# Kernel optimization log

Measured on AMD Instinct MI355X. Metric: run time of the kernel, lower is better.

The kernel has to match this reference:

```python
import jax, jax.numpy as jnp
import numpy as np

B, S, F, K = 64, 1024, 128, 64  # batch, seq(=l), feat(=d), bottleneck k


def setup_inputs() -> dict:
    key = jax.random.key(0)
    ks = jax.random.split(key, 24)
    r = lambda k_, sh, s=0.05: (jax.random.normal(k_, sh, dtype=jnp.float32) * s)
    inp = {
        'f1_norm': jax.random.normal(ks[0], (B, S, F), dtype=jnp.float32),
        'f2_norm': jax.random.normal(ks[1], (B, S, F), dtype=jnp.float32),
        'f3_norm': jax.random.normal(ks[2], (B, S, F), dtype=jnp.float32),
        # AMLP params (Linear(F, 2F))
        'Wi': r(ks[3], (2 * F, F)), 'bi': r(ks[4], (2 * F,)),
        'Wq': r(ks[5], (2 * F, F)), 'bq': r(ks[6], (2 * F,)),
        'Wvp': r(ks[7], (2 * F, F)), 'bvp': r(ks[8], (2 * F,)),
        # affine_{a,v,l}: Linear(l, l, bias=False) -> weight [l, l]
        'Aa': r(ks[9], (S, S)), 'Av': r(ks[10], (S, S)), 'Al': r(ks[11], (S, S)),
        # W_{a,v,t}: Linear(l, k) -> [k, l]
        'Wa': r(ks[12], (K, S)), 'Wv': r(ks[13], (K, S)), 'Wt': r(ks[14], (K, S)),
        # W_c{a,v,t}: Linear(2d, k) -> [k, 2F]
        'Wca': r(ks[15], (K, 2 * F)), 'Wcv': r(ks[16], (K, 2 * F)), 'Wct': r(ks[17], (K, 2 * F)),
        # W_h{a,v,t}: Linear(k, l) -> [l, k]
        'Wha': r(ks[18], (S, K)), 'Whv': r(ks[19], (S, K)), 'Wht': r(ks[20], (S, K)),
    }
    return inp


def _amlp(txt, aud, vis, Wi, bi, Wq, bq, Wvp, bvp):
    f1 = jnp.einsum('bsf,gf->bsg', txt, Wi) + bi  # [B,S,2F]
    f2 = jnp.einsum('bsf,gf->bsg', aud, Wq) + bq
    f3 = jnp.einsum('bsf,gf->bsg', vis, Wvp) + bvp
    n1 = jnp.linalg.norm(f1)
    n2 = jnp.linalg.norm(f2)
    n3 = jnp.linalg.norm(f3)
    # faithful to source: third term is scalar factor3 * norm3 (broadcast)
    exp_out = (n1 / (n1 + n2)) * f1 + (n2 / (n1 + n2)) * f2 + (n3 / (n1 + n2 + n3)) * n3
    b, s, g = exp_out.shape
    z = exp_out.reshape(b, s, g // 2, 2).sum(-1)  # AvgPool1d(2,2) * 2 == pair sum
    # F.normalize default dim=1 (over sequence axis for 3D tensor)
    z = z / jnp.maximum(jnp.linalg.norm(z, axis=1, keepdims=True), 1e-12)
    return z  # [B,S,F]


def reference(f1_norm, f2_norm, f3_norm, Wi, bi, Wq, bq, Wvp, bvp,
              Aa, Av, Al, Wa, Wv, Wt, Wca, Wcv, Wct, Wha, Whv, Wht):
    txt, aud, vis = f1_norm, f2_norm, f3_norm
    G = _amlp(txt, aud, vis, Wi, bi, Wq, bq, Wvp, bvp)  # [B,S,F]

    G_ag = jnp.concatenate([aud, G], axis=-1)  # [B,S,2F]
    G_vg = jnp.concatenate([vis, G], axis=-1)
    G_lg = jnp.concatenate([txt, G], axis=-1)
    scale = np.sqrt(G_ag.shape[-1]).astype(np.float32)  # sqrt(2F); same for all three

    # a_j = affine(G_xg^T); att = x^T @ a_j^T  ==  x^T @ (A @ G_xg)
    AGa = jnp.einsum('ts,bsc->btc', Aa, G_ag)
    C_a = jnp.tanh(jnp.einsum('bsf,bsc->bfc', aud, AGa) / scale)  # [B,F,2F]
    AGv = jnp.einsum('ts,bsc->btc', Av, G_ag)  # NOTE: source bug uses G_ag, not G_vg
    C_v = jnp.tanh(jnp.einsum('bsf,bsc->bfc', vis, AGv) / scale)
    AGl = jnp.einsum('ts,bsc->btc', Al, G_lg)
    C_t = jnp.tanh(jnp.einsum('bsf,bsc->bfc', txt, AGl) / scale)

    H_a = jax.nn.relu(jnp.einsum('bfc,kc->bfk', C_a, Wca) + jnp.einsum('bsf,ks->bfk', aud, Wa))
    H_v = jax.nn.relu(jnp.einsum('bfc,kc->bfk', C_v, Wcv) + jnp.einsum('bsf,ks->bfk', vis, Wv))
    H_t = jax.nn.relu(jnp.einsum('bfc,kc->bfk', C_t, Wct) + jnp.einsum('bsf,ks->bfk', txt, Wt))

    out_a = jnp.einsum('bfk,sk->bsf', H_a, Wha) + aud  # [B,S,F]
    out_v = jnp.einsum('bfk,sk->bsf', H_v, Whv) + vis
    out_t = jnp.einsum('bfk,sk->bsf', H_t, Wht) + txt
    return (out_t, out_a, out_v)
```

## Files before the change

### kernel.cpp

```cpp
#include <hip/hip_runtime.h>
#include <math.h>

constexpr int Bb = 64;
constexpr int Ss = 1024;
constexpr int Ff = 128;
constexpr int G2 = 256;
constexpr int Kk = 64;
constexpr int NE = 1152;

typedef __bf16 bfrag __attribute__((ext_vector_type(8)));
typedef float  facc  __attribute__((ext_vector_type(4)));
typedef short  s8v   __attribute__((ext_vector_type(8)));

__device__ __forceinline__ short f2bfs(float f) {
  union { float f; unsigned u; } v; v.f = f;
  unsigned r = v.u + 0x7FFFu + ((v.u >> 16) & 1u);
  return (short)(r >> 16);
}
__device__ __forceinline__ float bf2fs(short s) {
  union { unsigned u; float f; } v; v.u = ((unsigned)(unsigned short)s) << 16;
  return v.f;
}
__device__ __forceinline__ facc mfma16(bfrag a, bfrag b, facc c) {
  return __builtin_amdgcn_mfma_f32_16x16x32_bf16(a, b, c, 0, 0, 0);
}
__device__ __forceinline__ void gld16(const void* g, void* l) {
  __builtin_amdgcn_global_load_lds(
      (const __attribute__((address_space(1))) void*)g,
      (__attribute__((address_space(3))) void*)l, 16, 0, 0);
}

__global__ void k_transpose(const float* __restrict__ aud, const float* __restrict__ vis,
                            const float* __restrict__ txt, short* __restrict__ xT) {
  __shared__ float tile[64][65];
  int z = blockIdx.z;
  int mod = z >> 6, b = z & 63;
  const float* x = (mod == 0) ? aud : (mod == 1) ? vis : txt;
  int s0 = blockIdx.x * 64, f0 = blockIdx.y * 64;
  int tid = threadIdx.x;
  for (int i = 0; i < 16; ++i) {
    int idx = i * 256 + tid;
    int si = idx >> 6, fi = idx & 63;
    tile[si][fi] = x[((size_t)b * Ss + s0 + si) * Ff + f0 + fi];
  }
  __syncthreads();
  short* dst = xT + ((size_t)mod * Bb + b) * Ff * Ss;
  for (int i = 0; i < 16; ++i) {
    int idx = i * 256 + tid;
    int fi = idx >> 6, si = idx & 63;
    dst[(size_t)(f0 + fi) * Ss + s0 + si] = f2bfs(tile[si][fi]);
  }
}

__global__ void k_build_aextT(const float* __restrict__ Aa, const float* __restrict__ Av,
                              const float* __restrict__ Al, const float* __restrict__ Wa,
                              const float* __restrict__ Wv, const float* __restrict__ Wt,
                              short* __restrict__ aextT) {
  __shared__ float tile[64][65];
  int mod = blockIdx.z;
  const float* A = (mod == 0) ? Aa : (mod == 1) ? Av : Al;
  const float* W = (mod == 0) ? Wa : (mod == 1) ? Wv : Wt;
  short* dst = aextT + (size_t)mod * NE * Ss;
  int n0 = blockIdx.x * 64, t0 = blockIdx.y * 64;
  int tid = threadIdx.x;
  if (n0 < Ss) {
    for (int i = 0; i < 16; ++i) {
      int idx = i * 256 + tid;
      int ti = idx >> 6, nj = idx & 63;
      tile[ti][nj] = A[(size_t)(t0 + ti) * Ss + n0 + nj];
    }
    __syncthreads();
    for (int i = 0; i < 16; ++i) {
      int idx = i * 256 + tid;
      int nj = idx >> 6, ti = idx & 63;
      dst[(size_t)(n0 + nj) * Ss + t0 + ti] = f2bfs(tile[ti][nj]);
    }
  } else if (n0 < Ss + Kk) {
    for (int i = 0; i < 16; ++i) {
      int idx = i * 256 + tid;
      int j = idx >> 6, tt = idx & 63;
      dst[(size_t)(n0 + j) * Ss + t0 + tt] = f2bfs(W[(size_t)(n0 - Ss + j) * Ss + t0 + tt]);
    }
  } else {
    for (int i = 0; i < 16; ++i) {
      int idx = i * 256 + tid;
      int j = idx >> 6, tt = idx & 63;
      dst[(size_t)(n0 + j) * Ss + t0 + tt] = 0;
    }
  }
}

__global__ void k_build_w(const float* __restrict__ Wca, const float* __restrict__ Wcv,
                          const float* __restrict__ Wct, const float* __restrict__ Wha,
                          const float* __restrict__ Whv, const float* __restrict__ Wht,
                          const float* __restrict__ Wi, const float* __restrict__ Wq,
                          const float* __restrict__ Wvp,
                          short* __restrict__ wcb, short* __restrict__ whb,
                          short* __restrict__ wbar) {
  int idx = blockIdx.x * 256 + threadIdx.x;
  const int n1 = 3 * Kk * G2;
  const int n2 = n1 + 3 * Ss * Kk;
  if (idx < n1) {
    int mod = idx / (Kk * G2), r = idx - mod * (Kk * G2);
    const float* W = (mod == 0) ? Wca : (mod == 1) ? Wcv : Wct;
    wcb[idx] = f2bfs(W[r]);
  } else if (idx < n2) {
    int j = idx - n1;
    int mod = j / (Ss * Kk), r = j - mod * (Ss * Kk);
    const float* W = (mod == 0) ? Wha : (mod == 1) ? Whv : Wht;
    whb[j] = f2bfs(W[r]);
  } else {
    int j = idx - n2;
    int mod = j / (G2 * Ff), r = j - mod * (G2 * Ff);
    int n = r >> 7, k = r & 127;
    int t = n >> 4, nl = n & 15;
    int c = k >> 5, q = (k >> 3) & 3, e = k & 7;
    const float* W = (mod == 0) ? Wi : (mod == 1) ? Wq : Wvp;
    wbar[mod * G2 * Ff + (((t * 4 + c) * 64 + q * 16 + nl) * 8) + e] = f2bfs(W[r]);
  }
}

__global__ void __launch_bounds__(256, 3) k_amlp(
    const float* __restrict__ txt, const float* __restrict__ aud, const float* __restrict__ vis,
    const float* __restrict__ bi, const float* __restrict__ bq, const float* __restrict__ bvp,
    const short* __restrict__ wbar,
    short* __restrict__ p1, short* __restrict__ p2, float* __restrict__ sumsq) {
  int mod = blockIdx.y;
  const float* x    = (mod == 0) ? txt : (mod == 1) ? aud : vis;
  const float* bias = (mod == 0) ? bi  : (mod == 1) ? bq  : bvp;
  const short* wbm  = wbar + mod * G2 * Ff;
  short* pout = (mod == 0) ? p1 : (mod == 1) ? p2 : nullptr;

  __shared__ float wred[4];
  int tid = threadIdx.x, lane = tid & 63, wave = tid >> 6;
  int quad = lane >> 4, nl = lane & 15;

  bfrag wreg[4][4];
#pragma unroll
  for (int tt = 0; tt < 4; ++tt)
#pragma unroll
    for (int c = 0; c < 4; ++c)
      wreg[tt][c] = *(const bfrag*)(wbm + ((((wave * 4 + tt) * 4 + c) * 64 + lane) * 8));

  float bia[4];
#pragma unroll
  for (int tt = 0; tt < 4; ++tt) bia[tt] = bias[wave * 64 + tt * 16 + nl];

  const float* xblk = x + (size_t)(blockIdx.x * 256) * Ff;
  facc zero = {0.f, 0.f, 0.f, 0.f};
  float sq = 0.f;

  float4 buf[8];
  {
    const float* xrow = xblk + (size_t)nl * Ff;
#pragma unroll
    for (int c = 0; c < 4; ++c) {
      buf[c * 2]     = *(const float4*)(xrow + c * 32 + quad * 8);
      buf[c * 2 + 1] = *(const float4*)(xrow + c * 32 + quad * 8 + 4);
    }
  }

  for (int g = 0; g < 16; ++g) {
    bfrag af[4];
#pragma unroll
    for (int c = 0; c < 4; ++c) {
      float4 a0 = buf[c * 2], a1 = buf[c * 2 + 1];
      af[c][0] = (__bf16)a0.x; af[c][1] = (__bf16)a0.y;
      af[c][2] = (__bf16)a0.z; af[c][3] = (__bf16)a0.w;
      af[c][4] = (__bf16)a1.x; af[c][5] = (__bf16)a1.y;
      af[c][6] = (__bf16)a1.z; af[c][7] = (__bf16)a1.w;
    }
    if (g < 15) {
      const float* xrow = xblk + (size_t)((g + 1) * 16 + nl) * Ff;
#pragma unroll
      for (int c = 0; c < 4; ++c) {
        buf[c * 2]     = *(const float4*)(xrow + c * 32 + quad * 8);
        buf[c * 2 + 1] = *(const float4*)(xrow + c * 32 + quad * 8 + 4);
      }
    }
    facc acc[4];
#pragma unroll
    for (int tt = 0; tt < 4; ++tt) acc[tt] = zero;
#pragma unroll
    for (int c = 0; c < 4; ++c)
#pragma unroll
      for (int tt = 0; tt < 4; ++tt)
        acc[tt] = mfma16(af[c], wreg[tt][c], acc[tt]);

    int drow = blockIdx.x * 256 + g * 16 + quad * 4;
#pragma unroll
    for (int tt = 0; tt < 4; ++tt)
#pragma unroll
      for (int r = 0; r < 4; ++r) {
        float fv = acc[tt][r] + bia[tt];
        sq += fv * fv;
        if (pout) {
          float fo = fv + __shfl_xor(fv, 1, 64);
          if ((lane & 1) == 0)
            pout[(size_t)(drow + r) * Ff + wave * 32 + tt * 8 + (nl >> 1)] = f2bfs(fo);
        }
      }
  }
  for (int off = 32; off > 0; off >>= 1) sq += __shfl_down(sq, off, 64);
  if (lane == 0) wred[wave] = sq;
  __syncthreads();
  if (tid == 0) atomicAdd(&sumsq[mod], wred[0] + wred[1] + wred[2] + wred[3]);
}

__global__ void k_colnorm(const short* __restrict__ p1, const short* __restrict__ p2,
                          const float* __restrict__ sumsq, float* __restrict__ colnsq) {
  float n1 = sqrtf(sumsq[0]), n2 = sqrtf(sumsq[1]), n3 = sqrtf(sumsq[2]);
  float w1 = n1 / (n1 + n2), w2 = n2 / (n1 + n2);
  float tc = 2.f * n3 * n3 / (n1 + n2 + n3);
  int b = blockIdx.x, j = threadIdx.x;
  int s0 = blockIdx.y * 64;
  float a = 0.f;
  for (int s = s0; s < s0 + 64; ++s) {
    size_t off = ((size_t)b * Ss + s) * Ff + j;
    float z = w1 * bf2fs(p1[off]) + w2 * bf2fs(p2[off]) + tc;
    a += z * z;
  }
  atomicAdd(&colnsq[b * Ff + j], a);
}

__global__ void k_gnormT(const short* __restrict__ p1, const short* __restrict__ p2,
                         const float* __restrict__ sumsq, const float* __restrict__ colnsq,
                         short* __restrict__ gT) {
  __shared__ float tile[64][65];
  float n1 = sqrtf(sumsq[0]), n2 = sqrtf(sumsq[1]), n3 = sqrtf(sumsq[2]);
  float w1 = n1 / (n1 + n2), w2 = n2 / (n1 + n2);
  float tc = 2.f * n3 * n3 / (n1 + n2 + n3);
  int b = blockIdx.z, s0 = blockIdx.x * 64, f0 = blockIdx.y * 64;
  int tid = threadIdx.x;
  for (int i = 0; i < 16; ++i) {
    int idx = i * 256 + tid;
    int si = idx >> 6, fi = idx & 63;
    size_t off = ((size_t)b * Ss + s0 + si) * Ff + f0 + fi;
    float z = w1 * bf2fs(p1[off]) + w2 * bf2fs(p2[off]) + tc;
    float cn = fmaxf(sqrtf(colnsq[b * Ff + f0 + fi]), 1e-12f);
    tile[si][fi] = z / cn;
  }
  __syncthreads();
  short* dst = gT + (size_t)b * Ff * Ss;
  for (int i = 0; i < 16; ++i) {
    int idx = i * 256 + tid;
    int fi = idx >> 6, si = idx & 63;
    dst[(size_t)(f0 + fi) * Ss + s0 + si] = f2bfs(tile[si][fi]);
  }
}

__global__ void __launch_bounds__(256) k_mgemm(const short* __restrict__ xT,
                                               const short* __restrict__ aextT,
                                               short* __restrict__ mxext) {
  int mod = blockIdx.z;
  const short* Ap = xT + (size_t)mod * Bb * Ff * Ss;
  const short* Bp = aextT + (size_t)mod * NE * Ss;
  short* Op = mxext + (size_t)mod * Bb * Ff * NE;
  int M0 = blockIdx.x * 128, N0 = blockIdx.y * 128;
  __shared__ short As[128 * 64];
  __shared__ short Bs[128 * 64];
  int tid = threadIdx.x, lane = tid & 63, wave = tid >> 6;
  int quad = lane >> 4, nl = lane & 15;
  int wm = (wave >> 1) * 64, wn = (wave & 1) * 64;
  facc zero = {0.f, 0.f, 0.f, 0.f};
  facc acc[4][4];
  for (int i = 0; i < 4; ++i) for (int j = 0; j < 4; ++j) acc[i][j] = zero;
  for (int k0 = 0; k0 < Ss; k0 += 64) {
    __syncthreads();
#pragma unroll
    for (int i = 0; i < 4; ++i) {
      int idx = i * 256 + tid;
      int r = idx >> 3, cs = ((idx & 7) ^ (r & 7)) * 8;
      gld16(Ap + (size_t)(M0 + r) * Ss + k0 + cs, As + idx * 8);
      gld16(Bp + (size_t)(N0 + r) * Ss + k0 + cs, Bs + idx * 8);
    }
    __syncthreads();
#pragma unroll
    for (int kc = 0; kc < 2; ++kc) {
      bfrag a[4], bfr[4];
      for (int mt = 0; mt < 4; ++mt) {
        int row = wm + mt * 16 + nl;
        a[mt] = *(const bfrag*)(As + row * 64 + (((kc * 4 + quad) ^ (row & 7)) * 8));
      }
      for (int nt = 0; nt < 4; ++nt) {
        int row = wn + nt * 16 + nl;
        bfr[nt] = *(const bfrag*)(Bs + row * 64 + (((kc * 4 + quad) ^ (row & 7)) * 8));
      }
      for (int mt = 0; mt < 4; ++mt)
        for (int nt = 0; nt < 4; ++nt)
          acc[mt][nt] = mfma16(a[mt], bfr[nt], acc[mt][nt]);
    }
  }
  for (int mt = 0; mt < 4; ++mt)
    for (int nt = 0; nt < 4; ++nt)
      for (int r = 0; r < 4; ++r) {
        int row = M0 + wm + mt * 16 + quad * 4 + r;
        int col = N0 + wn + nt * 16 + nl;
        Op[(size_t)row * NE + col] = f2bfs(acc[mt][nt][r]);
      }
}

__global__ void __launch_bounds__(512) k_chgemm(const short* __restrict__ mxext,
                                                const short* __restrict__ xT,
                                                const short* __restrict__ gT,
                                                const short* __restrict__ wcb,
                                                short* __restrict__ h) {
  int b = blockIdx.x, mod = blockIdx.y;
  const short* Ap = mxext + ((size_t)mod * Bb + b) * Ff * NE;
  const short* xTb = xT + (size_t)((mod == 2) ? 2 : 0) * Bb * Ff * Ss + (size_t)b * Ff * Ss;
  const short* gTb = gT + (size_t)b * Ff * Ss;
  const short* Wp = wcb + (size_t)mod * Kk * G2;
  short* Hp = h + ((size_t)mod * Bb + b) * Ff * Kk;

  __shared__ short smem[128 * 272];
  short* As = smem;
  short* Bs = smem + 128 * 64;

  int tid = threadIdx.x, lane = tid & 63, wave = tid >> 6;
  int quad = lane >> 4, nl = lane & 15;
  int wm = (wave >> 2) * 64, wn = (wave & 3) * 64;
  facc zero = {0.f, 0.f, 0.f, 0.f};
  facc acc[4][4];
  for (int i = 0; i < 4; ++i) for (int j = 0; j < 4; ++j) acc[i][j] = zero;
  for (int k0 = 0; k0 < Ss; k0 += 64) {
    __syncthreads();
#pragma unroll
    for (int i = 0; i < 2; ++i) {
      int idx = i * 512 + tid;
      int r = idx >> 3, cs = ((idx & 7) ^ (r & 7)) * 8;
      gld16(Ap + (size_t)r * NE + k0 + cs, As + idx * 8);
    }
#pragma unroll
    for (int i = 0; i < 4; ++i) {
      int idx = i * 512 + tid;
      int r = idx >> 3, cs = ((idx & 7) ^ (r & 7)) * 8;
      const short* src = (r < 128) ? (xTb + (size_t)r * Ss) : (gTb + (size_t)(r - 128) * Ss);
      gld16(src + k0 + cs, Bs + idx * 8);
    }
    __syncthreads();
#pragma unroll
    for (int kc = 0; kc < 2; ++kc) {
      bfrag a[4], bfr[4];
      for (int mt = 0; mt < 4; ++mt) {
        int row = wm + mt * 16 + nl;
        a[mt] = *(const bfrag*)(As + row * 64 + (((kc * 4 + quad) ^ (row & 7)) * 8));
      }
      for (int nt = 0; nt < 4; ++nt) {
        int row = wn + nt * 16 + nl;
        bfr[nt] = *(const bfrag*)(Bs + row * 64 + (((kc * 4 + quad) ^ (row & 7)) * 8));
      }
      for (int mt = 0; mt < 4; ++mt)
        for (int nt = 0; nt < 4; ++nt)
          acc[mt][nt] = mfma16(a[mt], bfr[nt], acc[mt][nt]);
    }
  }
  __syncthreads();
  short* Cs = smem;
  for (int mt = 0; mt < 4; ++mt)
    for (int nt = 0; nt < 4; ++nt)
      for (int r = 0; r < 4; ++r) {
        int row = wm + mt * 16 + quad * 4 + r;
        int col = wn + nt * 16 + nl;
        Cs[row * 272 + col] = f2bfs(tanhf(acc[mt][nt][r] * 0.0625f));
      }
  __syncthreads();
  facc hacc[4];
  for (int nt = 0; nt < 4; ++nt) hacc[nt] = zero;
  for (int k0 = 0; k0 < G2; k0 += 32) {
    bfrag ca = *(const bfrag*)(Cs + (wave * 16 + nl) * 272 + k0 + quad * 8);
    for (int nt = 0; nt < 4; ++nt) {
      bfrag wb = *(const bfrag*)(Wp + (size_t)(nt * 16 + nl) * G2 + k0 + quad * 8);
      hacc[nt] = mfma16(ca, wb, hacc[nt]);
    }
  }
  for (int nt = 0; nt < 4; ++nt)
    for (int r = 0; r < 4; ++r) {
      int row = wave * 16 + quad * 4 + r;
      int col = nt * 16 + nl;
      float v = hacc[nt][r] + bf2fs(Ap[(size_t)row * NE + Ss + col]);
      Hp[(size_t)row * Kk + col] = f2bfs(fmaxf(v, 0.f));
    }
}

__global__ void k_outgemm(const short* __restrict__ whb, const short* __restrict__ h,
                          const float* __restrict__ txt, const float* __restrict__ aud,
                          const float* __restrict__ vis, float* __restrict__ outp) {
  int s0 = blockIdx.x * 128, b = blockIdx.y, mod = blockIdx.z;
  const short* Wp = whb + (size_t)mod * Ss * Kk;
  const short* Hp = h + ((size_t)mod * Bb + b) * Ff * Kk;
  const float* xres = ((mod == 0) ? aud : (mod == 1) ? vis : txt) + (size_t)b * Ss * Ff;
  int slot = (mod == 0) ? 1 : (mod == 1) ? 2 : 0;
  float* Op = outp + ((size_t)slot * Bb + b) * Ss * Ff;
  int tid = threadIdx.x, lane = tid & 63, wave = tid >> 6;
  int quad = lane >> 4, nl = lane & 15;
  int wm = (wave >> 1) * 64, wn = (wave & 1) * 64;
  facc zero = {0.f, 0.f, 0.f, 0.f};
  facc acc[4][4];
  for (int i = 0; i < 4; ++i) for (int j = 0; j < 4; ++j) acc[i][j] = zero;
  for (int k0 = 0; k0 < Kk; k0 += 32) {
    bfrag a[4], bfr[4];
    for (int mt = 0; mt < 4; ++mt)
      a[mt] = *(const bfrag*)(Wp + (size_t)(s0 + wm + mt * 16 + nl) * Kk + k0 + quad * 8);
    for (int nt = 0; nt < 4; ++nt)
      bfr[nt] = *(const bfrag*)(Hp + (size_t)(wn + nt * 16 + nl) * Kk + k0 + quad * 8);
    for (int mt = 0; mt < 4; ++mt)
      for (int nt = 0; nt < 4; ++nt)
        acc[mt][nt] = mfma16(a[mt], bfr[nt], acc[mt][nt]);
  }
  for (int mt = 0; mt < 4; ++mt)
    for (int nt = 0; nt < 4; ++nt)
      for (int r = 0; r < 4; ++r) {
        int srow = s0 + wm + mt * 16 + quad * 4 + r;
        int col = wn + nt * 16 + nl;
        size_t o = (size_t)srow * Ff + col;
        Op[o] = acc[mt][nt][r] + xres[o];
      }
}

extern "C" void kernel_launch(void* const* d_in, const int* in_sizes, int n_in,
                              void* d_out, int out_size, void* d_ws, size_t ws_size,
                              hipStream_t stream) {
  const float* txt = (const float*)d_in[0];
  const float* aud = (const float*)d_in[1];
  const float* vis = (const float*)d_in[2];
  const float* Wi  = (const float*)d_in[3];
  const float* bi  = (const float*)d_in[4];
  const float* Wq  = (const float*)d_in[5];
  const float* bq  = (const float*)d_in[6];
  const float* Wvp = (const float*)d_in[7];
  const float* bvp = (const float*)d_in[8];
  const float* Aa  = (const float*)d_in[9];
  const float* Av  = (const float*)d_in[10];
  const float* Al  = (const float*)d_in[11];
  const float* Wa  = (const float*)d_in[12];
  const float* Wv  = (const float*)d_in[13];
  const float* Wt  = (const float*)d_in[14];
  const float* Wca = (const float*)d_in[15];
  const float* Wcv = (const float*)d_in[16];
  const float* Wct = (const float*)d_in[17];
  const float* Wha = (const float*)d_in[18];
  const float* Whv = (const float*)d_in[19];
  const float* Wht = (const float*)d_in[20];

  char* w = (char*)d_ws;
  float* sumsq  = (float*)w;
  float* colnsq = (float*)(w + 256);
  size_t off = 65536;
  short* xT    = (short*)(w + off); off += (size_t)3 * Bb * Ff * Ss * 2;
  short* aextT = (short*)(w + off); off += (size_t)3 * NE * Ss * 2;
  short* gT    = (short*)(w + off); off += (size_t)Bb * Ff * Ss * 2;
  short* mx    = (short*)(w + off);
  short* p1    = mx;
  short* p2    = mx + (size_t)Bb * Ss * Ff;
  off += (size_t)3 * Bb * Ff * NE * 2;
  short* h     = (short*)(w + off); off += (size_t)3 * Bb * Ff * Kk * 2;
  short* wcb   = (short*)(w + off); off += (size_t)3 * Kk * G2 * 2;
  short* whb   = (short*)(w + off); off += (size_t)3 * Ss * Kk * 2;
  short* wbar  = (short*)(w + off); off += (size_t)3 * G2 * Ff * 2;

  hipMemsetAsync(d_ws, 0, 65536, stream);
  k_transpose<<<dim3(16, 2, 192), 256, 0, stream>>>(aud, vis, txt, xT);
  k_build_aextT<<<dim3(NE / 64, 16, 3), 256, 0, stream>>>(Aa, Av, Al, Wa, Wv, Wt, aextT);
  k_build_w<<<(3 * Kk * G2 + 3 * Ss * Kk + 3 * G2 * Ff) / 256, 256, 0, stream>>>(
      Wca, Wcv, Wct, Wha, Whv, Wht, Wi, Wq, Wvp, wcb, whb, wbar);
  k_amlp<<<dim3(Bb * Ss / 256, 3), 256, 0, stream>>>(txt, aud, vis, bi, bq, bvp,
                                                     wbar, p1, p2, sumsq);
  k_colnorm<<<dim3(Bb, 16), 128, 0, stream>>>(p1, p2, sumsq, colnsq);
  k_gnormT<<<dim3(16, 2, Bb), 256, 0, stream>>>(p1, p2, sumsq, colnsq, gT);
  k_mgemm<<<dim3(Bb * Ff / 128, NE / 128, 3), 256, 0, stream>>>(xT, aextT, mx);
  k_chgemm<<<dim3(Bb, 3), 512, 0, stream>>>(mx, xT, gT, wcb, h);
  k_outgemm<<<dim3(Ss / 128, Bb, 3), 256, 0, stream>>>(whb, h, txt, aud, vis, (float*)d_out);
}
```

Before: 458.3 us.

## Double-buffer k_mgemm LDS loads and split k_chgemm rows across two blocks

After: 450.6 us. No clear change (-1.7%).

```diff
diff --git a/kernel.cpp b/kernel.cpp
--- a/kernel.cpp
+++ b/kernel.cpp
@@ -249,47 +249,67 @@
   }
 }
 
-__global__ void __launch_bounds__(256) k_mgemm(const short* __restrict__ xT,
-                                               const short* __restrict__ aextT,
-                                               short* __restrict__ mxext) {
+__device__ __forceinline__ void stage_mg(const short* Ap, const short* Bp,
+                                         short* As, short* Bs,
+                                         int tid, int M0, int N0, int k0) {
+#pragma unroll
+  for (int i = 0; i < 4; ++i) {
+    int idx = i * 256 + tid;
+    int r = idx >> 3, cs = ((idx & 7) ^ (r & 7)) * 8;
+    gld16(Ap + (size_t)(M0 + r) * Ss + k0 + cs, As + idx * 8);
+    gld16(Bp + (size_t)(N0 + r) * Ss + k0 + cs, Bs + idx * 8);
+  }
+}
+
+__global__ void __launch_bounds__(256, 2) k_mgemm(const short* __restrict__ xT,
+                                                  const short* __restrict__ aextT,
+                                                  short* __restrict__ mxext) {
   int mod = blockIdx.z;
   const short* Ap = xT + (size_t)mod * Bb * Ff * Ss;
   const short* Bp = aextT + (size_t)mod * NE * Ss;
   short* Op = mxext + (size_t)mod * Bb * Ff * NE;
   int M0 = blockIdx.x * 128, N0 = blockIdx.y * 128;
-  __shared__ short As[128 * 64];
-  __shared__ short Bs[128 * 64];
+  __shared__ short As[2][128 * 64];
+  __shared__ short Bs[2][128 * 64];
   int tid = threadIdx.x, lane = tid & 63, wave = tid >> 6;
   int quad = lane >> 4, nl = lane & 15;
   int wm = (wave >> 1) * 64, wn = (wave & 1) * 64;
   facc zero = {0.f, 0.f, 0.f, 0.f};
   facc acc[4][4];
   for (int i = 0; i < 4; ++i) for (int j = 0; j < 4; ++j) acc[i][j] = zero;
-  for (int k0 = 0; k0 < Ss; k0 += 64) {
-    __syncthreads();
-#pragma unroll
-    for (int i = 0; i < 4; ++i) {
-      int idx = i * 256 + tid;
-      int r = idx >> 3, cs = ((idx & 7) ^ (r & 7)) * 8;
-      gld16(Ap + (size_t)(M0 + r) * Ss + k0 + cs, As + idx * 8);
-      gld16(Bp + (size_t)(N0 + r) * Ss + k0 + cs, Bs + idx * 8);
-    }
-    __syncthreads();
+
+  stage_mg(Ap, Bp, As[0], Bs[0], tid, M0, N0, 0);
+  stage_mg(Ap, Bp, As[1], Bs[1], tid, M0, N0, 64);
+
+  for (int t = 0; t < 16; ++t) {
+    int cur = t & 1;
+    if (t < 15) { asm volatile("s_waitcnt vmcnt(8)" ::: "memory"); }
+    else        { asm volatile("s_waitcnt vmcnt(0)" ::: "memory"); }
+    __builtin_amdgcn_s_barrier();
+    __builtin_amdgcn_sched_barrier(0);
+    const short* Asb = As[cur];
+    const short* Bsb = Bs[cur];
 #pragma unroll
     for (int kc = 0; kc < 2; ++kc) {
       bfrag a[4], bfr[4];
       for (int mt = 0; mt < 4; ++mt) {
         int row = wm + mt * 16 + nl;
-        a[mt] = *(const bfrag*)(As + row * 64 + (((kc * 4 + quad) ^ (row & 7)) * 8));
+        a[mt] = *(const bfrag*)(Asb + row * 64 + (((kc * 4 + quad) ^ (row & 7)) * 8));
       }
       for (int nt = 0; nt < 4; ++nt) {
         int row = wn + nt * 16 + nl;
-        bfr[nt] = *(const bfrag*)(Bs + row * 64 + (((kc * 4 + quad) ^ (row & 7)) * 8));
+        bfr[nt] = *(const bfrag*)(Bsb + row * 64 + (((kc * 4 + quad) ^ (row & 7)) * 8));
       }
       for (int mt = 0; mt < 4; ++mt)
         for (int nt = 0; nt < 4; ++nt)
           acc[mt][nt] = mfma16(a[mt], bfr[nt], acc[mt][nt]);
     }
+    __builtin_amdgcn_sched_barrier(0);
+    asm volatile("s_waitcnt lgkmcnt(0)" ::: "memory");
+    __builtin_amdgcn_s_barrier();
+    __builtin_amdgcn_sched_barrier(0);
+    if (t < 14)
+      stage_mg(Ap, Bp, As[cur], Bs[cur], tid, M0, N0, (t + 2) * 64);
   }
   for (int mt = 0; mt < 4; ++mt)
     for (int nt = 0; nt < 4; ++nt)
@@ -300,25 +320,26 @@
       }
 }
 
-__global__ void __launch_bounds__(512) k_chgemm(const short* __restrict__ mxext,
+__global__ void __launch_bounds__(256) k_chgemm(const short* __restrict__ mxext,
                                                 const short* __restrict__ xT,
                                                 const short* __restrict__ gT,
                                                 const short* __restrict__ wcb,
                                                 short* __restrict__ h) {
-  int b = blockIdx.x, mod = blockIdx.y;
+  int b = blockIdx.x, mod = blockIdx.y, half = blockIdx.z;
+  int r0 = half * 64;
   const short* Ap = mxext + ((size_t)mod * Bb + b) * Ff * NE;
   const short* xTb = xT + (size_t)((mod == 2) ? 2 : 0) * Bb * Ff * Ss + (size_t)b * Ff * Ss;
   const short* gTb = gT + (size_t)b * Ff * Ss;
   const short* Wp = wcb + (size_t)mod * Kk * G2;
   short* Hp = h + ((size_t)mod * Bb + b) * Ff * Kk;
 
-  __shared__ short smem[128 * 272];
+  __shared__ short smem[64 * 64 + 256 * 64];
   short* As = smem;
-  short* Bs = smem + 128 * 64;
+  short* Bs = smem + 64 * 64;
 
   int tid = threadIdx.x, lane = tid & 63, wave = tid >> 6;
   int quad = lane >> 4, nl = lane & 15;
-  int wm = (wave >> 2) * 64, wn = (wave & 3) * 64;
+  int wn = wave * 64;
   facc zero = {0.f, 0.f, 0.f, 0.f};
   facc acc[4][4];
   for (int i = 0; i < 4; ++i) for (int j = 0; j < 4; ++j) acc[i][j] = zero;
@@ -326,13 +347,13 @@
     __syncthreads();
 #pragma unroll
     for (int i = 0; i < 2; ++i) {
-      int idx = i * 512 + tid;
+      int idx = i * 256 + tid;
       int r = idx >> 3, cs = ((idx & 7) ^ (r & 7)) * 8;
-      gld16(Ap + (size_t)r * NE + k0 + cs, As + idx * 8);
-    }
-#pragma unroll
-    for (int i = 0; i < 4; ++i) {
-      int idx = i * 512 + tid;
+      gld16(Ap + (size_t)(r0 + r) * NE + k0 + cs, As + idx * 8);
+    }
+#pragma unroll
+    for (int i = 0; i < 8; ++i) {
+      int idx = i * 256 + tid;
       int r = idx >> 3, cs = ((idx & 7) ^ (r & 7)) * 8;
       const short* src = (r < 128) ? (xTb + (size_t)r * Ss) : (gTb + (size_t)(r - 128) * Ss);
       gld16(src + k0 + cs, Bs + idx * 8);
@@ -342,7 +363,7 @@
     for (int kc = 0; kc < 2; ++kc) {
       bfrag a[4], bfr[4];
       for (int mt = 0; mt < 4; ++mt) {
-        int row = wm + mt * 16 + nl;
+        int row = mt * 16 + nl;
         a[mt] = *(const bfrag*)(As + row * 64 + (((kc * 4 + quad) ^ (row & 7)) * 8));
       }
       for (int nt = 0; nt < 4; ++nt) {
@@ -359,7 +380,7 @@
   for (int mt = 0; mt < 4; ++mt)
     for (int nt = 0; nt < 4; ++nt)
       for (int r = 0; r < 4; ++r) {
-        int row = wm + mt * 16 + quad * 4 + r;
+        int row = mt * 16 + quad * 4 + r;
         int col = wn + nt * 16 + nl;
         Cs[row * 272 + col] = f2bfs(tanhf(acc[mt][nt][r] * 0.0625f));
       }
@@ -375,7 +396,7 @@
   }
   for (int nt = 0; nt < 4; ++nt)
     for (int r = 0; r < 4; ++r) {
-      int row = wave * 16 + quad * 4 + r;
+      int row = r0 + wave * 16 + quad * 4 + r;
       int col = nt * 16 + nl;
       float v = hacc[nt][r] + bf2fs(Ap[(size_t)row * NE + Ss + col]);
       Hp[(size_t)row * Kk + col] = f2bfs(fmaxf(v, 0.f));
@@ -468,6 +489,6 @@
   k_colnorm<<<dim3(Bb, 16), 128, 0, stream>>>(p1, p2, sumsq, colnsq);
   k_gnormT<<<dim3(16, 2, Bb), 256, 0, stream>>>(p1, p2, sumsq, colnsq, gT);
   k_mgemm<<<dim3(Bb * Ff / 128, NE / 128, 3), 256, 0, stream>>>(xT, aextT, mx);
-  k_chgemm<<<dim3(Bb, 3), 512, 0, stream>>>(mx, xT, gT, wcb, h);
+  k_chgemm<<<dim3(Bb, 3, 2), 256, 0, stream>>>(mx, xT, gT, wcb, h);
   k_outgemm<<<dim3(Ss / 128, Bb, 3), 256, 0, stream>>>(whb, h, txt, aud, vis, (float*)d_out);
 }
```

## Split channel GEMM across two row-half blocks and vectorize transpose stores

Applied to the files above, without the earlier changes.

After: 446.6 us. 2.6% less time.

```diff
diff --git a/kernel.cpp b/kernel.cpp
--- a/kernel.cpp
+++ b/kernel.cpp
@@ -11,6 +11,7 @@
 typedef __bf16 bfrag __attribute__((ext_vector_type(8)));
 typedef float  facc  __attribute__((ext_vector_type(4)));
 typedef short  s8v   __attribute__((ext_vector_type(8)));
+typedef short  s4v   __attribute__((ext_vector_type(4)));
 
 __device__ __forceinline__ short f2bfs(float f) {
   union { float f; unsigned u; } v; v.f = f;
@@ -38,17 +39,32 @@
   const float* x = (mod == 0) ? aud : (mod == 1) ? vis : txt;
   int s0 = blockIdx.x * 64, f0 = blockIdx.y * 64;
   int tid = threadIdx.x;
-  for (int i = 0; i < 16; ++i) {
-    int idx = i * 256 + tid;
-    int si = idx >> 6, fi = idx & 63;
-    tile[si][fi] = x[((size_t)b * Ss + s0 + si) * Ff + f0 + fi];
+  {
+    int fg = tid & 15, sb = tid >> 4;
+#pragma unroll
+    for (int i = 0; i < 4; ++i) {
+      int si = i * 16 + sb;
+      float4 v = *(const float4*)(x + ((size_t)b * Ss + s0 + si) * Ff + f0 + fg * 4);
+      tile[si][fg * 4 + 0] = v.x;
+      tile[si][fg * 4 + 1] = v.y;
+      tile[si][fg * 4 + 2] = v.z;
+      tile[si][fg * 4 + 3] = v.w;
+    }
   }
   __syncthreads();
   short* dst = xT + ((size_t)mod * Bb + b) * Ff * Ss;
-  for (int i = 0; i < 16; ++i) {
-    int idx = i * 256 + tid;
-    int fi = idx >> 6, si = idx & 63;
-    dst[(size_t)(f0 + fi) * Ss + s0 + si] = f2bfs(tile[si][fi]);
+  {
+    int sg = tid & 15, fb = tid >> 4;
+#pragma unroll
+    for (int i = 0; i < 4; ++i) {
+      int fi = i * 16 + fb;
+      s4v v;
+      v[0] = f2bfs(tile[sg * 4 + 0][fi]);
+      v[1] = f2bfs(tile[sg * 4 + 1][fi]);
+      v[2] = f2bfs(tile[sg * 4 + 2][fi]);
+      v[3] = f2bfs(tile[sg * 4 + 3][fi]);
+      *(s4v*)(dst + (size_t)(f0 + fi) * Ss + s0 + sg * 4) = v;
+    }
   }
 }
 
@@ -70,10 +86,16 @@
       tile[ti][nj] = A[(size_t)(t0 + ti) * Ss + n0 + nj];
     }
     __syncthreads();
-    for (int i = 0; i < 16; ++i) {
-      int idx = i * 256 + tid;
-      int nj = idx >> 6, ti = idx & 63;
-      dst[(size_t)(n0 + nj) * Ss + t0 + ti] = f2bfs(tile[ti][nj]);
+    int tg = tid & 15, nb = tid >> 4;
+#pragma unroll
+    for (int i = 0; i < 4; ++i) {
+      int nj = i * 16 + nb;
+      s4v v;
+      v[0] = f2bfs(tile[tg * 4 + 0][nj]);
+      v[1] = f2bfs(tile[tg * 4 + 1][nj]);
+      v[2] = f2bfs(tile[tg * 4 + 2][nj]);
+      v[3] = f2bfs(tile[tg * 4 + 3][nj]);
+      *(s4v*)(dst + (size_t)(n0 + nj) * Ss + t0 + tg * 4) = v;
     }
   } else if (n0 < Ss + Kk) {
     for (int i = 0; i < 16; ++i) {
@@ -227,25 +249,36 @@
                          const float* __restrict__ sumsq, const float* __restrict__ colnsq,
                          short* __restrict__ gT) {
   __shared__ float tile[64][65];
+  __shared__ float invcn[64];
   float n1 = sqrtf(sumsq[0]), n2 = sqrtf(sumsq[1]), n3 = sqrtf(sumsq[2]);
   float w1 = n1 / (n1 + n2), w2 = n2 / (n1 + n2);
   float tc = 2.f * n3 * n3 / (n1 + n2 + n3);
   int b = blockIdx.z, s0 = blockIdx.x * 64, f0 = blockIdx.y * 64;
   int tid = threadIdx.x;
+  if (tid < 64)
+    invcn[tid] = 1.f / fmaxf(sqrtf(colnsq[b * Ff + f0 + tid]), 1e-12f);
+  __syncthreads();
   for (int i = 0; i < 16; ++i) {
     int idx = i * 256 + tid;
     int si = idx >> 6, fi = idx & 63;
     size_t off = ((size_t)b * Ss + s0 + si) * Ff + f0 + fi;
     float z = w1 * bf2fs(p1[off]) + w2 * bf2fs(p2[off]) + tc;
-    float cn = fmaxf(sqrtf(colnsq[b * Ff + f0 + fi]), 1e-12f);
-    tile[si][fi] = z / cn;
+    tile[si][fi] = z * invcn[fi];
   }
   __syncthreads();
   short* dst = gT + (size_t)b * Ff * Ss;
-  for (int i = 0; i < 16; ++i) {
-    int idx = i * 256 + tid;
-    int fi = idx >> 6, si = idx & 63;
-    dst[(size_t)(f0 + fi) * Ss + s0 + si] = f2bfs(tile[si][fi]);
+  {
+    int sg = tid & 15, fb = tid >> 4;
+#pragma unroll
+    for (int i = 0; i < 4; ++i) {
+      int fi = i * 16 + fb;
+      s4v v;
+      v[0] = f2bfs(tile[sg * 4 + 0][fi]);
+      v[1] = f2bfs(tile[sg * 4 + 1][fi]);
+      v[2] = f2bfs(tile[sg * 4 + 2][fi]);
+      v[3] = f2bfs(tile[sg * 4 + 3][fi]);
+      *(s4v*)(dst + (size_t)(f0 + fi) * Ss + s0 + sg * 4) = v;
+    }
   }
 }
 
@@ -300,25 +333,26 @@
       }
 }
 
-__global__ void __launch_bounds__(512) k_chgemm(const short* __restrict__ mxext,
+__global__ void __launch_bounds__(256) k_chgemm(const short* __restrict__ mxext,
                                                 const short* __restrict__ xT,
                                                 const short* __restrict__ gT,
                                                 const short* __restrict__ wcb,
                                                 short* __restrict__ h) {
-  int b = blockIdx.x, mod = blockIdx.y;
+  int b = blockIdx.x, mod = blockIdx.y, half = blockIdx.z;
+  int r0 = half * 64;
   const short* Ap = mxext + ((size_t)mod * Bb + b) * Ff * NE;
   const short* xTb = xT + (size_t)((mod == 2) ? 2 : 0) * Bb * Ff * Ss + (size_t)b * Ff * Ss;
   const short* gTb = gT + (size_t)b * Ff * Ss;
   const short* Wp = wcb + (size_t)mod * Kk * G2;
   short* Hp = h + ((size_t)mod * Bb + b) * Ff * Kk;
 
-  __shared__ short smem[128 * 272];
+  __shared__ short smem[64 * 64 + 256 * 64];
   short* As = smem;
-  short* Bs = smem + 128 * 64;
+  short* Bs = smem + 64 * 64;
 
   int tid = threadIdx.x, lane = tid & 63, wave = tid >> 6;
   int quad = lane >> 4, nl = lane & 15;
-  int wm = (wave >> 2) * 64, wn = (wave & 3) * 64;
+  int wn = wave * 64;
   facc zero = {0.f, 0.f, 0.f, 0.f};
   facc acc[4][4];
   for (int i = 0; i < 4; ++i) for (int j = 0; j < 4; ++j) acc[i][j] = zero;
@@ -326,13 +360,13 @@
     __syncthreads();
 #pragma unroll
     for (int i = 0; i < 2; ++i) {
-      int idx = i * 512 + tid;
+      int idx = i * 256 + tid;
       int r = idx >> 3, cs = ((idx & 7) ^ (r & 7)) * 8;
-      gld16(Ap + (size_t)r * NE + k0 + cs, As + idx * 8);
-    }
-#pragma unroll
-    for (int i = 0; i < 4; ++i) {
-      int idx = i * 512 + tid;
+      gld16(Ap + (size_t)(r0 + r) * NE + k0 + cs, As + idx * 8);
+    }
+#pragma unroll
+    for (int i = 0; i < 8; ++i) {
+      int idx = i * 256 + tid;
       int r = idx >> 3, cs = ((idx & 7) ^ (r & 7)) * 8;
       const short* src = (r < 128) ? (xTb + (size_t)r * Ss) : (gTb + (size_t)(r - 128) * Ss);
       gld16(src + k0 + cs, Bs + idx * 8);
@@ -342,7 +376,7 @@
     for (int kc = 0; kc < 2; ++kc) {
       bfrag a[4], bfr[4];
       for (int mt = 0; mt < 4; ++mt) {
-        int row = wm + mt * 16 + nl;
+        int row = mt * 16 + nl;
         a[mt] = *(const bfrag*)(As + row * 64 + (((kc * 4 + quad) ^ (row & 7)) * 8));
       }
       for (int nt = 0; nt < 4; ++nt) {
@@ -359,7 +393,7 @@
   for (int mt = 0; mt < 4; ++mt)
     for (int nt = 0; nt < 4; ++nt)
       for (int r = 0; r < 4; ++r) {
-        int row = wm + mt * 16 + quad * 4 + r;
+        int row = mt * 16 + quad * 4 + r;
         int col = wn + nt * 16 + nl;
         Cs[row * 272 + col] = f2bfs(tanhf(acc[mt][nt][r] * 0.0625f));
       }
@@ -375,7 +409,7 @@
   }
   for (int nt = 0; nt < 4; ++nt)
     for (int r = 0; r < 4; ++r) {
-      int row = wave * 16 + quad * 4 + r;
+      int row = r0 + wave * 16 + quad * 4 + r;
       int col = nt * 16 + nl;
       float v = hacc[nt][r] + bf2fs(Ap[(size_t)row * NE + Ss + col]);
       Hp[(size_t)row * Kk + col] = f2bfs(fmaxf(v, 0.f));
@@ -468,6 +502,6 @@
   k_colnorm<<<dim3(Bb, 16), 128, 0, stream>>>(p1, p2, sumsq, colnsq);
   k_gnormT<<<dim3(16, 2, Bb), 256, 0, stream>>>(p1, p2, sumsq, colnsq, gT);
   k_mgemm<<<dim3(Bb * Ff / 128, NE / 128, 3), 256, 0, stream>>>(xT, aextT, mx);
-  k_chgemm<<<dim3(Bb, 3), 512, 0, stream>>>(mx, xT, gT, wcb, h);
+  k_chgemm<<<dim3(Bb, 3, 2), 256, 0, stream>>>(mx, xT, gT, wcb, h);
   k_outgemm<<<dim3(Ss / 128, Bb, 3), 256, 0, stream>>>(whb, h, txt, aud, vis, (float*)d_out);
 }
```
